# Kernel optimization log

Measured on AMD Instinct MI355X. Metric: run time of the kernel, lower is better.

Reference implementation:

```python
import jax, jax.numpy as jnp
import numpy as np

BINS = 10


def setup_inputs() -> dict:
    key = jax.random.key(0)
    k1, k2 = jax.random.split(key)
    pred = jax.random.normal(k1, (16384, 4096), dtype=jnp.float32)
    target = jax.random.randint(k2, (16384, 4096), 0, 2).astype(jnp.float32)
    return {"pred": pred, "target": target}


def reference(pred, target):
    bins = BINS
    # edges = [0, 0.1, ..., 1.0], last edge bumped by 1e-6 (as in torch module)
    edges = jnp.arange(bins + 1, dtype=jnp.float32) / bins
    edges = edges.at[-1].add(1e-6)

    # gradient magnitude g = |pred.detach() - target|
    g = jnp.abs(jax.lax.stop_gradient(pred) - target)

    # label_weight is forced to all-ones in the original forward -> all valid
    tot = jnp.float32(g.size)

    # histogram binning: element e belongs to bin i iff edges[i] <= g < edges[i+1]
    gf = g.ravel()
    idx = jnp.searchsorted(edges, gf, side="right") - 1  # in [-1, bins]
    in_range = (idx >= 0) & (idx < bins)                  # g >= 1+1e-6 falls outside
    idxc = jnp.clip(idx, 0, bins - 1)
    counts = jnp.zeros(bins, jnp.float32).at[idxc].add(in_range.astype(jnp.float32))

    n = jnp.sum(counts > 0).astype(jnp.float32)  # number of non-empty bins
    cnt_e = counts[idxc]                          # per-element bin count
    per = jnp.where(in_range & (cnt_e > 0), tot / jnp.maximum(cnt_e, 1.0), 0.0)
    weights = (per / jnp.maximum(n, 1.0)).reshape(pred.shape)

    # weighted BCE with logits, reduction='sum', normalized by tot
    log_p = jax.nn.log_sigmoid(pred)
    log_np = jax.nn.log_sigmoid(-pred)
    loss = -jnp.sum(weights * (target * log_p + (1.0 - target) * log_np)) / tot
    return loss
```

## Files before the change

kernel.cpp:

```cpp
#include <hip/hip_runtime.h>


#define THREADS 256
#define NB 10
#define PF 4

__device__ __forceinline__ float bce(float x, float t) {
    return fmaxf(x, 0.0f) - x * t + __logf(1.0f + __expf(-fabsf(x)));
}

__global__ __launch_bounds__(THREADS) void ghmc_partial(
    const float4* __restrict__ p4, const float4* __restrict__ t4, int n4,
    const float* __restrict__ p1, const float* __restrict__ t1, long long ntot,
    double* __restrict__ g_sum, unsigned int* __restrict__ g_cnt) {

    const int tid = threadIdx.x;

    const float EDGE10 = 1.0f + 1e-6f;
    unsigned long long cc[4] = {0ull, 0ull, 0ull, 0ull};
    unsigned cnt[NB];
    float acc[NB];
#pragma unroll
    for (int b = 0; b < NB; ++b) { cnt[b] = 0u; acc[b] = 0.0f; }

    auto put = [&](float x, float t, unsigned long long& c) {
        const float g = fabsf(x - t);
        const float l = bce(x, t);
        int idx = (int)(g * 10.0f);
        idx = idx > 9 ? 9 : idx;
        idx = (g < EDGE10) ? idx : 10;
        c += 1ull << (6 * idx);
#pragma unroll
        for (int b = 0; b < NB; ++b)
            acc[b] += (idx == b) ? l : 0.0f;
    };
    auto flush_all = [&]() {
#pragma unroll
        for (int q = 0; q < 4; ++q) {
#pragma unroll
            for (int b = 0; b < NB; ++b)
                cnt[b] += (unsigned)((cc[q] >> (6 * b)) & 63ull);
            cc[q] = 0ull;
        }
    };

    const int chunk = (n4 + (int)gridDim.x - 1) / (int)gridDim.x;
    const int start = blockIdx.x * chunk;
    const int end = min(start + chunk, n4);
    const int count = max(end - start, 0);
    const int full = count / THREADS;
    const int ngrp = full / PF;

    float4 PA[PF], TA[PF], PB[PF], TB[PF];
    auto loadg = [&](float4 (&Pd)[PF], float4 (&Td)[PF], int grp) {
#pragma unroll
        for (int g = 0; g < PF; ++g) {
            const int id = start + grp * PF * THREADS + g * THREADS + tid;
            Pd[g] = p4[id]; Td[g] = t4[id];
        }
    };
    auto proc = [&](float4 (&Pd)[PF], float4 (&Td)[PF]) {
#pragma unroll
        for (int g = 0; g < PF; ++g) {
            put(Pd[g].x, Td[g].x, cc[0]);
            put(Pd[g].y, Td[g].y, cc[1]);
            put(Pd[g].z, Td[g].z, cc[2]);
            put(Pd[g].w, Td[g].w, cc[3]);
        }
    };

    int fcnt = 0;
    if (ngrp > 0) loadg(PA, TA, 0);
    int g2 = 0;
    for (; g2 + 2 <= ngrp; g2 += 2) {
        loadg(PB, TB, g2 + 1);
        proc(PA, TA);
        if (g2 + 2 < ngrp) loadg(PA, TA, g2 + 2);
        proc(PB, TB);
        fcnt += 2 * PF;
        if (fcnt >= 56) { flush_all(); fcnt = 0; }
    }
    if (g2 < ngrp) proc(PA, TA);

    for (int k = ngrp * PF; k < full; ++k) {
        const int id = start + k * THREADS + tid;
        const float4 pp = p4[id], tt = t4[id];
        put(pp.x, tt.x, cc[0]); put(pp.y, tt.y, cc[1]);
        put(pp.z, tt.z, cc[2]); put(pp.w, tt.w, cc[3]);
    }
    {
        const int id = start + full * THREADS + tid;
        if (id < end) {
            const float4 pp = p4[id], tt = t4[id];
            put(pp.x, tt.x, cc[0]); put(pp.y, tt.y, cc[1]);
            put(pp.z, tt.z, cc[2]); put(pp.w, tt.w, cc[3]);
        }
    }
    flush_all();

    if (blockIdx.x == 0 && tid == 0) {
        for (long long j = (long long)n4 * 4; j < ntot; ++j) {
            const float x = p1[j], tt = t1[j];
            const float g = fabsf(x - tt);
            if (g < EDGE10) {
                int idx = (int)(g * 10.0f);
                idx = idx > 9 ? 9 : idx;
                atomicAdd(&g_sum[idx], (double)bce(x, tt));
                atomicAdd(&g_cnt[idx], 1u);
            }
        }
    }

#pragma unroll
    for (int off = 32; off > 0; off >>= 1) {
#pragma unroll
        for (int b = 0; b < NB; ++b) {
            acc[b] += __shfl_down(acc[b], off, 64);
            cnt[b] += __shfl_down(cnt[b], off, 64);
        }
    }

    __shared__ float w_sum[4][NB];
    __shared__ unsigned w_cnt[4][NB];
    const int wave = tid >> 6;
    const int lane = tid & 63;
    if (lane == 0) {
#pragma unroll
        for (int b = 0; b < NB; ++b) { w_sum[wave][b] = acc[b]; w_cnt[wave][b] = cnt[b]; }
    }
    __syncthreads();
    if (tid < NB) {
        const float fs = w_sum[0][tid] + w_sum[1][tid] + w_sum[2][tid] + w_sum[3][tid];
        const unsigned fc = w_cnt[0][tid] + w_cnt[1][tid] + w_cnt[2][tid] + w_cnt[3][tid];
        atomicAdd(&g_sum[tid], (double)fs);
        atomicAdd(&g_cnt[tid], fc);
    }
}

__global__ void ghmc_final(const double* __restrict__ g_sum,
                           const unsigned int* __restrict__ g_cnt,
                           float* __restrict__ out) {
    if (blockIdx.x == 0 && threadIdx.x == 0) {
        double loss = 0.0;
        int n = 0;
#pragma unroll
        for (int b = 0; b < NB; ++b) {
            const unsigned c = g_cnt[b];
            if (c > 0u) {
                n += 1;
                loss += g_sum[b] / (double)c;
            }
        }
        loss /= (n > 0) ? (double)n : 1.0;
        out[0] = (float)loss;
    }
}

extern "C" void kernel_launch(void* const* d_in, const int* in_sizes, int n_in,
                              void* d_out, int out_size, void* d_ws, size_t ws_size,
                              hipStream_t stream) {
    const float* pred = (const float*)d_in[0];
    const float* tgt  = (const float*)d_in[1];
    long long ntot = (long long)in_sizes[0];
    int n4 = (int)(ntot / 4);

    double* g_sum = (double*)d_ws;
    unsigned int* g_cnt = (unsigned int*)((char*)d_ws + NB * sizeof(double));

    hipMemsetAsync(d_ws, 0, NB * sizeof(double) + NB * sizeof(unsigned int),
                   stream);

    const int threads = THREADS;
    const int blocks = 2048;
    hipLaunchKernelGGL(ghmc_partial, dim3(blocks), dim3(threads), 0, stream,
                       (const float4*)pred, (const float4*)tgt, n4,
                       pred, tgt, ntot, g_sum, g_cnt);
    hipLaunchKernelGGL(ghmc_final, dim3(1), dim3(64), 0, stream,
                       g_sum, g_cnt, (float*)d_out);
}
```

Measured before the change: 526.4 us.

## Replace double-buffered prefetch with simple 2-way unrolled loop and raise occupancy

Removes the register-heavy double-buffered PF=4 prefetch scheme and replaces it with a plain loop that loads two float4 pairs per iteration. It also adds a launch-bounds minimum-blocks hint of 8 so the compiler limits register use and more waves can be resident. Latency hiding now depends on having more waves in flight rather than on explicit software prefetch. Each thread issues fewer loads ahead, so if occupancy does not actually rise the memory pipeline may stall more.

```diff
diff --git a/kernel.cpp b/kernel.cpp
--- a/kernel.cpp
+++ b/kernel.cpp
@@ -3,13 +3,12 @@
 
 #define THREADS 256
 #define NB 10
-#define PF 4
 
 __device__ __forceinline__ float bce(float x, float t) {
     return fmaxf(x, 0.0f) - x * t + __logf(1.0f + __expf(-fabsf(x)));
 }
 
-__global__ __launch_bounds__(THREADS) void ghmc_partial(
+__global__ __launch_bounds__(THREADS, 8) void ghmc_partial(
     const float4* __restrict__ p4, const float4* __restrict__ t4, int n4,
     const float* __restrict__ p1, const float* __restrict__ t1, long long ntot,
     double* __restrict__ g_sum, unsigned int* __restrict__ g_cnt) {
@@ -49,40 +48,21 @@
     const int end = min(start + chunk, n4);
     const int count = max(end - start, 0);
     const int full = count / THREADS;
-    const int ngrp = full / PF;
 
-    float4 PA[PF], TA[PF], PB[PF], TB[PF];
-    auto loadg = [&](float4 (&Pd)[PF], float4 (&Td)[PF], int grp) {
-#pragma unroll
-        for (int g = 0; g < PF; ++g) {
-            const int id = start + grp * PF * THREADS + g * THREADS + tid;
-            Pd[g] = p4[id]; Td[g] = t4[id];
-        }
-    };
-    auto proc = [&](float4 (&Pd)[PF], float4 (&Td)[PF]) {
-#pragma unroll
-        for (int g = 0; g < PF; ++g) {
-            put(Pd[g].x, Td[g].x, cc[0]);
-            put(Pd[g].y, Td[g].y, cc[1]);
-            put(Pd[g].z, Td[g].z, cc[2]);
-            put(Pd[g].w, Td[g].w, cc[3]);
-        }
-    };
-
-    int fcnt = 0;
-    if (ngrp > 0) loadg(PA, TA, 0);
-    int g2 = 0;
-    for (; g2 + 2 <= ngrp; g2 += 2) {
-        loadg(PB, TB, g2 + 1);
-        proc(PA, TA);
-        if (g2 + 2 < ngrp) loadg(PA, TA, g2 + 2);
-        proc(PB, TB);
-        fcnt += 2 * PF;
-        if (fcnt >= 56) { flush_all(); fcnt = 0; }
+    int k = 0;
+    int since = 0;
+    for (; k + 2 <= full; k += 2) {
+        const int id0 = start + k * THREADS + tid;
+        const int id1 = id0 + THREADS;
+        const float4 pa = p4[id0], ta = t4[id0];
+        const float4 pb = p4[id1], tb = t4[id1];
+        put(pa.x, ta.x, cc[0]); put(pa.y, ta.y, cc[1]);
+        put(pa.z, ta.z, cc[2]); put(pa.w, ta.w, cc[3]);
+        put(pb.x, tb.x, cc[0]); put(pb.y, tb.y, cc[1]);
+        put(pb.z, tb.z, cc[2]); put(pb.w, tb.w, cc[3]);
+        if (++since >= 28) { flush_all(); since = 0; }
     }
-    if (g2 < ngrp) proc(PA, TA);
-
-    for (int k = ngrp * PF; k < full; ++k) {
+    for (; k < full; ++k) {
         const int id = start + k * THREADS + tid;
         const float4 pp = p4[id], tt = t4[id];
         put(pp.x, tt.x, cc[0]); put(pp.y, tt.y, cc[1]);
```

After: 576.3 us. +9.5%, slower.
